# Optimization experiments

Measured on AMD Instinct MI355X. Metric: run time of the kernel, lower is better.

Reference implementation:

```python
import jax, jax.numpy as jnp
import numpy as np

B, N, DIM, H = 8, 1024, 768, 12
D = DIM // H  # head_dim = 64
SCALE = D ** -0.5


def setup_inputs() -> dict:
    key = jax.random.key(0)
    k1, k2, k3, k4 = jax.random.split(key, 4)
    x = jax.random.normal(k1, (B, N, DIM), dtype=jnp.float32)
    # nn.Linear(dim, dim*3, bias=False): weight [3*dim, dim]; y = x @ W^T
    w_qkv = jax.random.normal(k2, (3 * DIM, DIM), dtype=jnp.float32) * (DIM ** -0.5)
    # nn.Linear(dim, dim) with bias
    w_proj = jax.random.normal(k3, (DIM, DIM), dtype=jnp.float32) * (DIM ** -0.5)
    b_proj = jax.random.normal(k4, (DIM,), dtype=jnp.float32) * 0.01
    return {"x": x, "w_qkv": w_qkv, "w_proj": w_proj, "b_proj": b_proj}


def reference(x, w_qkv, w_proj, b_proj):
    b, n, dim = x.shape
    qkv = x @ w_qkv.T  # [b, n, 3*dim]
    # rearrange 'b n (h d qkv) -> qkv b h n d' (qkv innermost in the split)
    qkv = qkv.reshape(b, n, H, D, 3)
    qkv = jnp.transpose(qkv, (4, 0, 2, 1, 3))  # [3, b, h, n, d]
    q, k, v = qkv[0], qkv[1], qkv[2]
    energy = jnp.einsum('bhqd,bhkd->bhqk', q, k) * SCALE
    att = jax.nn.softmax(energy, axis=-1)  # dropout p=0.0 -> identity
    out = jnp.einsum('bhal,bhlv->bhav', att, v)  # [b, h, n, d]
    out = jnp.transpose(out, (0, 2, 1, 3)).reshape(b, n, dim)
    return out @ w_proj.T + b_proj
```

## Files before the change

kernel.cpp:

```cpp
#include <hip/hip_runtime.h>
#include <hip/hip_bf16.h>
#include <stdint.h>

#define NH 12

typedef __attribute__((ext_vector_type(8))) short bf16x8;
typedef __attribute__((ext_vector_type(4))) float f32x4;

static __device__ __forceinline__ ushort f2bf(float f) {
  union { float f; uint32_t u; } v; v.f = f;
  uint32_t r = (v.u + 0x7FFFu + ((v.u >> 16) & 1u)) >> 16;
  return (ushort)r;
}

static __device__ __forceinline__ uint32_t cvtpk(float lo, float hi) {
  uint32_t r;
  asm("v_cvt_pk_bf16_f32 %0, %1, %2" : "=v"(r) : "v"(lo), "v"(hi));
  return r;
}

static __device__ __forceinline__ void gl_lds16(const void* g, void* l) {
  __builtin_amdgcn_global_load_lds(
      (const __attribute__((address_space(1))) uint32_t*)(uintptr_t)g,
      (__attribute__((address_space(3))) uint32_t*)(uintptr_t)l,
      16, 0, 0);
}

static __device__ __forceinline__ f32x4 mfma32(bf16x8 a, bf16x8 b, f32x4 c) {
  return __builtin_amdgcn_mfma_f32_16x16x32_bf16(a, b, c, 0, 0, 0);
}

#define QSCALE 0.1803368801111601f

__global__ __launch_bounds__(256) void k_cvt(const float4* __restrict__ src,
                                             ushort4* __restrict__ dst, int n4) {
  int i = blockIdx.x * blockDim.x + threadIdx.x;
  if (i < n4) {
    float4 v = src[i];
    ushort4 o;
    o.x = f2bf(v.x); o.y = f2bf(v.y); o.z = f2bf(v.z); o.w = f2bf(v.w);
    dst[i] = o;
  }
}

__global__ __launch_bounds__(256) void k_cvt_wq(const float4* __restrict__ src,
                                                ushort4* __restrict__ dst) {
  int i = blockIdx.x * 256 + threadIdx.x;
  if (i >= 2304 * 192) return;
  int ro = i / 192, cc = i - ro * 192;
  int h = ro / 192;
  int rem = ro - h * 192;
  int d = rem / 3;
  int which = rem - d * 3;
  int rn = which * 768 + h * 64 + d;
  float4 v = src[i];
  ushort4 o;
  o.x = f2bf(v.x); o.y = f2bf(v.y); o.z = f2bf(v.z); o.w = f2bf(v.w);
  dst[(size_t)rn * 192 + cc] = o;
}

#define DECL_GEMM_VARS() \
  const int tid = threadIdx.x; \
  const int w = tid >> 6, l = tid & 63, g = l >> 4, c15 = l & 15; \
  const int wm = w >> 1, wn = w & 1; \
  const int dst0 = w * 1024 + l * 16; \
  const int row_s = w * 16 + (l >> 2); \
  const int cg = ((l & 3) ^ ((l >> 3) & 3)) * 8; \
  const int gsw = (g ^ ((c15 >> 1) & 3)) * 8;

#define STAGE(pa, pb, Aptr, Bptr, kk0) do { \
    gl_lds16((Aptr) + (size_t)(m0 + row_s) * 768 + (kk0) + cg, (char*)(pa) + dst0); \
    gl_lds16((Aptr) + (size_t)(m0 + row_s + 64) * 768 + (kk0) + cg, (char*)(pa) + dst0 + 4096); \
    gl_lds16((Bptr) + (size_t)(n0 + row_s) * 768 + (kk0) + cg, (char*)(pb) + dst0); \
    gl_lds16((Bptr) + (size_t)(n0 + row_s + 64) * 768 + (kk0) + cg, (char*)(pb) + dst0 + 4096); \
  } while (0)

#define COMPUTE(pa, pb) do { \
    bf16x8 af[4], bfr[4]; \
    _Pragma("unroll") \
    for (int i = 0; i < 4; i++) { \
      af[i]  = *(const bf16x8*)&(pa)[(wm * 64 + i * 16 + c15) * 32 + gsw]; \
      bfr[i] = *(const bf16x8*)&(pb)[(wn * 64 + i * 16 + c15) * 32 + gsw]; \
    } \
    _Pragma("unroll") \
    for (int mr = 0; mr < 4; mr++) \
      _Pragma("unroll") \
      for (int nr = 0; nr < 4; nr++) \
        acc[mr][nr] = mfma32(af[mr], bfr[nr], acc[mr][nr]); \
  } while (0)

#define WB4 do { __builtin_amdgcn_sched_barrier(0); \
    asm volatile("s_waitcnt vmcnt(4)\n\ts_barrier" ::: "memory"); \
    __builtin_amdgcn_sched_barrier(0); } while (0)
#define WB0 do { __builtin_amdgcn_sched_barrier(0); \
    asm volatile("s_waitcnt vmcnt(0)\n\ts_barrier" ::: "memory"); \
    __builtin_amdgcn_sched_barrier(0); } while (0)
#define PFENCE do { asm volatile("" ::: "memory"); \
    __builtin_amdgcn_sched_barrier(0); } while (0)

#define GEMM_PIPE(Aptr, Bptr) do { \
    STAGE(A0, B0, Aptr, Bptr, 0); \
    PFENCE; \
    STAGE(A1, B1, Aptr, Bptr, 32); \
    WB4; \
    _Pragma("unroll 1") \
    for (int k0 = 0; k0 < 672; k0 += 96) { \
      STAGE(A2, B2, Aptr, Bptr, k0 + 64);  COMPUTE(A0, B0); WB4; \
      STAGE(A0, B0, Aptr, Bptr, k0 + 96);  COMPUTE(A1, B1); WB4; \
      STAGE(A1, B1, Aptr, Bptr, k0 + 128); COMPUTE(A2, B2); WB4; \
    } \
    STAGE(A2, B2, Aptr, Bptr, 736); COMPUTE(A0, B0); WB4; \
    COMPUTE(A1, B1); WB0; \
    COMPUTE(A2, B2); \
  } while (0)

__global__ __launch_bounds__(256, 3) void k_qkv(const ushort* __restrict__ X,
                                                const ushort* __restrict__ W,
                                                ushort* __restrict__ Qb,
                                                ushort* __restrict__ Kf,
                                                ushort* __restrict__ Vf) {
  __shared__ __align__(16) ushort lds[24576];
  const int id = (int)blockIdx.x;
  const int swz = (id & 7) * 144 + (id >> 3);
  const int bx = swz % 18, by = swz / 18;
  const int m0 = by * 128, n0 = bx * 128;
  DECL_GEMM_VARS();

  ushort* A0 = lds;
  ushort* A1 = lds + 4096;
  ushort* A2 = lds + 8192;
  ushort* B0 = lds + 12288;
  ushort* B1 = lds + 16384;
  ushort* B2 = lds + 20480;

  f32x4 acc[4][4] = {};
  GEMM_PIPE(X, W);
  __syncthreads();

  const int type = bx / 6;
  const int cb = (bx % 6) * 128;
  const int h0 = cb >> 6;
  const int b = m0 >> 10, nbase = m0 & 1023, tbase = nbase >> 5;

  if (type == 0) {
#pragma unroll
    for (int nr = 0; nr < 4; nr++) {
      const int colrel = wn * 64 + nr * 16 + c15;
#pragma unroll
      for (int mr = 0; mr < 4; mr++)
#pragma unroll
        for (int r = 0; r < 4; r++) {
          const int mrel = wm * 64 + mr * 16 + 4 * g + r;
          lds[mrel * 128 + colrel] = f2bf(acc[mr][nr][r] * QSCALE);
        }
    }
    __syncthreads();
#pragma unroll
    for (int j = 0; j < 8; j++) {
      const int cid = j * 256 + tid;
      const int n = cid >> 4, coloff = (cid & 15) * 8;
      const int hrel = coloff >> 6, d0q = coloff & 63;
      bf16x8 vv = *(const bf16x8*)&lds[n * 128 + coloff];
      *(bf16x8*)(Qb + ((size_t)(b * NH + h0 + hrel) * 1024 + nbase + n) * 64 + d0q) = vv;
    }
  } else if (type == 1) {
#pragma unroll
    for (int nr = 0; nr < 4; nr++) {
      const int colrel = wn * 64 + nr * 16 + c15;
      const int hrel = colrel >> 6, d = colrel & 63;
      const int gk = (d >> 3) & 3, ek = d & 7, hi = d >> 5;
#pragma unroll
      for (int mr = 0; mr < 4; mr++)
#pragma unroll
        for (int r = 0; r < 4; r++) {
          const int mrel = wm * 64 + mr * 16 + 4 * g + r;
          const int trel = mrel >> 5, kk = mrel & 31;
          const int x = kk >> 3, s = (kk >> 2) & 1, y = kk & 3;
          lds[(hrel * 4 + trel) * 2048 + (2 * s + hi) * 512 +
              (gk * 16 + x * 4 + y) * 8 + ek] = f2bf(acc[mr][nr][r]);
        }
    }
    __syncthreads();
    const int c = tid >> 5, jj = tid & 31;
    ushort* dst = Kf + ((size_t)(b * NH + h0 + (c >> 2)) * 32 + tbase + (c & 3)) * 2048;
    const ushort* srcl = lds + c * 2048;
#pragma unroll
    for (int k2 = 0; k2 < 8; k2++)
      *(bf16x8*)(dst + jj * 8 + k2 * 256) = *(const bf16x8*)(srcl + jj * 8 + k2 * 256);
  } else {
#pragma unroll
    for (int nr = 0; nr < 4; nr++) {
      const int colrel = wn * 64 + nr * 16 + c15;
      const int hrel = colrel >> 6, d = colrel & 63;
      const int dtv = d >> 4, cv = d & 15;
#pragma unroll
      for (int mr = 0; mr < 4; mr++)
#pragma unroll
        for (int r = 0; r < 4; r++) {
          const int mrel = wm * 64 + mr * 16 + 4 * g + r;
          const int trel = mrel >> 5, kk = mrel & 31;
          const int gv = kk >> 3, ev = kk & 7;
          lds[(hrel * 4 + trel) * 2048 + dtv * 512 +
              (gv * 16 + cv) * 8 + ev] = f2bf(acc[mr][nr][r]);
        }
    }
    __syncthreads();
    const int c = tid >> 5, jj = tid & 31;
    ushort* dst = Vf + ((size_t)(b * NH + h0 + (c >> 2)) * 32 + tbase + (c & 3)) * 2048;
    const ushort* srcl = lds + c * 2048;
#pragma unroll
    for (int k2 = 0; k2 < 8; k2++)
      *(bf16x8*)(dst + jj * 8 + k2 * 256) = *(const bf16x8*)(srcl + jj * 8 + k2 * 256);
  }
}

__global__ __launch_bounds__(256, 3) void k_attn(const ushort* __restrict__ Qb,
                                                 const ushort* __restrict__ Kf,
                                                 const ushort* __restrict__ Vf,
                                                 ushort* __restrict__ Ab) {
  const int bh = blockIdx.x;
  const int tid = threadIdx.x;
  const int w = tid >> 6, l = tid & 63, g = l >> 4, c15 = l & 15;
  const int q0 = blockIdx.y * 128 + w * 32;

  bf16x8 qf0a, qf0b, qf1a, qf1b;
  {
    const ushort* qp = Qb + ((size_t)bh * 1024 + q0 + c15) * 64 + g * 8;
    qf0a = *(const bf16x8*)qp;
    qf0b = *(const bf16x8*)(qp + 32);
    qf1a = *(const bf16x8*)(qp + 1024);
    qf1b = *(const bf16x8*)(qp + 1024 + 32);
  }
  const ushort* kfb = Kf + (size_t)bh * 32 * 2048 + l * 8;
  const ushort* vfb = Vf + (size_t)bh * 32 * 2048 + l * 8;

  bf16x8 vones;
#pragma unroll
  for (int j = 0; j < 8; j++) vones[j] = (short)0x3F80;

  f32x4 o0[4] = {}, o1[4] = {};
  f32x4 ol0 = {}, ol1 = {};

  bf16x8 kA[4], vA[4], kB[4], vB[4];
#pragma unroll
  for (int j = 0; j < 4; j++) {
    kA[j] = *(const bf16x8*)(kfb + j * 512);
    vA[j] = *(const bf16x8*)(vfb + j * 512);
  }

#define ATT_BODY(KK, VV) do { \
    f32x4 s00 = {0.f,0.f,0.f,0.f}, s01 = {0.f,0.f,0.f,0.f}; \
    f32x4 s10 = {0.f,0.f,0.f,0.f}, s11 = {0.f,0.f,0.f,0.f}; \
    s00 = mfma32(KK[0], qf0a, s00); s00 = mfma32(KK[1], qf0b, s00); \
    s01 = mfma32(KK[0], qf1a, s01); s01 = mfma32(KK[1], qf1b, s01); \
    s10 = mfma32(KK[2], qf0a, s10); s10 = mfma32(KK[3], qf0b, s10); \
    s11 = mfma32(KK[2], qf1a, s11); s11 = mfma32(KK[3], qf1b, s11); \
    float p0[8], p1[8]; \
    _Pragma("unroll") \
    for (int r = 0; r < 4; r++) { \
      p0[r]     = exp2f(s00[r]); \
      p0[4 + r] = exp2f(s10[r]); \
      p1[r]     = exp2f(s01[r]); \
      p1[4 + r] = exp2f(s11[r]); \
    } \
    union { uint32_t u[4]; bf16x8 v; } pa0, pa1; \
    _Pragma("unroll") \
    for (int j = 0; j < 4; j++) { \
      pa0.u[j] = cvtpk(p0[2 * j], p0[2 * j + 1]); \
      pa1.u[j] = cvtpk(p1[2 * j], p1[2 * j + 1]); \
    } \
    ol0 = mfma32(pa0.v, vones, ol0); \
    ol1 = mfma32(pa1.v, vones, ol1); \
    _Pragma("unroll") \
    for (int dt = 0; dt < 4; dt++) { \
      o0[dt] = mfma32(pa0.v, VV[dt], o0[dt]); \
      o1[dt] = mfma32(pa1.v, VV[dt], o1[dt]); \
    } \
  } while (0)

#pragma unroll 1
  for (int t = 0; t < 32; t += 2) {
    {
      const ushort* kp = kfb + (t + 1) * 2048;
      const ushort* vp = vfb + (t + 1) * 2048;
#pragma unroll
      for (int j = 0; j < 4; j++) {
        kB[j] = *(const bf16x8*)(kp + j * 512);
        vB[j] = *(const bf16x8*)(vp + j * 512);
      }
    }
    ATT_BODY(kA, vA);
    {
      const int tn = (t + 2 < 32) ? (t + 2) : 31;
      const ushort* kp = kfb + tn * 2048;
      const ushort* vp = vfb + tn * 2048;
#pragma unroll
      for (int j = 0; j < 4; j++) {
        kA[j] = *(const bf16x8*)(kp + j * 512);
        vA[j] = *(const bf16x8*)(vp + j * 512);
      }
    }
    ATT_BODY(kB, vB);
  }
#undef ATT_BODY

  float il0[4], il1[4];
#pragma unroll
  for (int r = 0; r < 4; r++) {
    il0[r] = __builtin_amdgcn_rcpf(ol0[r]);
    il1[r] = __builtin_amdgcn_rcpf(ol1[r]);
  }
  const int b = bh / NH, h = bh % NH;
#pragma unroll
  for (int dt = 0; dt < 4; dt++)
#pragma unroll
    for (int r = 0; r < 4; r++) {
      const int n = q0 + 4 * g + r;
      Ab[(size_t)(b * 1024 + n) * 768 + h * 64 + dt * 16 + c15] =
          f2bf(o0[dt][r] * il0[r]);
      Ab[(size_t)(b * 1024 + n + 16) * 768 + h * 64 + dt * 16 + c15] =
          f2bf(o1[dt][r] * il1[r]);
    }
}

__global__ __launch_bounds__(256, 3) void k_proj(const ushort* __restrict__ Ain,
                                                 const ushort* __restrict__ W,
                                                 const float* __restrict__ Bp,
                                                 float* __restrict__ Out) {
  __shared__ __align__(16) ushort lds[24576];
  const int id = (int)blockIdx.x;
  const int swz = (id & 7) * 48 + (id >> 3);
  const int bx = swz % 6, by = swz / 6;
  const int m0 = by * 128, n0 = bx * 128;
  DECL_GEMM_VARS();

  ushort* A0 = lds;
  ushort* A1 = lds + 4096;
  ushort* A2 = lds + 8192;
  ushort* B0 = lds + 12288;
  ushort* B1 = lds + 16384;
  ushort* B2 = lds + 20480;

  f32x4 acc[4][4] = {};
  GEMM_PIPE(Ain, W);

#pragma unroll
  for (int nr = 0; nr < 4; nr++) {
    const int cc = n0 + wn * 64 + nr * 16 + c15;
    const float bias = Bp[cc];
#pragma unroll
    for (int mr = 0; mr < 4; mr++) {
      const int mb = m0 + wm * 64 + mr * 16 + 4 * g;
#pragma unroll
      for (int r = 0; r < 4; r++) {
        const int m = mb + r;
        Out[(size_t)m * 768 + cc] = acc[mr][nr][r] + bias;
      }
    }
  }
}

extern "C" void kernel_launch(void* const* d_in, const int* in_sizes, int n_in,
                              void* d_out, int out_size, void* d_ws, size_t ws_size,
                              hipStream_t stream) {
  const float* X  = (const float*)d_in[0];
  const float* Wq = (const float*)d_in[1];
  const float* Wp = (const float*)d_in[2];
  const float* Bp = (const float*)d_in[3];
  float* Out = (float*)d_out;

  char* ws = (char*)d_ws;
  const size_t SZ = (size_t)96 * 1024 * 64 * sizeof(ushort);
  ushort* Qb  = (ushort*)(ws);
  ushort* Kf  = (ushort*)(ws + SZ);
  ushort* Vf  = (ushort*)(ws + 2 * SZ);
  ushort* Ab  = (ushort*)(ws + 3 * SZ);
  ushort* Xb  = (ushort*)(ws + 4 * SZ);
  ushort* Wqb = (ushort*)(ws + 5 * SZ);
  ushort* Wpb = (ushort*)(ws + 5 * SZ + 2304 * 768 * 2);

  const int nX = 8192 * 768 / 4, nWp = 768 * 768 / 4;
  k_cvt<<<(nX + 255) / 256, 256, 0, stream>>>((const float4*)X, (ushort4*)Xb, nX);
  k_cvt_wq<<<(2304 * 192 + 255) / 256, 256, 0, stream>>>((const float4*)Wq, (ushort4*)Wqb);
  k_cvt<<<(nWp + 255) / 256, 256, 0, stream>>>((const float4*)Wp, (ushort4*)Wpb, nWp);

  k_qkv<<<1152, 256, 0, stream>>>(Xb, Wqb, Qb, Kf, Vf);
  k_attn<<<dim3(96, 8), 256, 0, stream>>>(Qb, Kf, Vf, Ab);
  k_proj<<<384, 256, 0, stream>>>(Ab, Wpb, Bp, Out);
}
```

Measured before the change: 133.1 us.

## Share K/V tiles via LDS triple buffer in attention and fuse conversion kernels

```diff
diff --git a/kernel.cpp b/kernel.cpp
--- a/kernel.cpp
+++ b/kernel.cpp
@@ -32,31 +32,40 @@
 
 #define QSCALE 0.1803368801111601f
 
-__global__ __launch_bounds__(256) void k_cvt(const float4* __restrict__ src,
-                                             ushort4* __restrict__ dst, int n4) {
-  int i = blockIdx.x * blockDim.x + threadIdx.x;
-  if (i < n4) {
-    float4 v = src[i];
+#define N4_X  1572864
+#define N4_WQ 442368
+#define N4_WP 147456
+__global__ __launch_bounds__(256) void k_cvt_all(const float4* __restrict__ X,
+                                                 const float4* __restrict__ Wq,
+                                                 const float4* __restrict__ Wp,
+                                                 ushort4* __restrict__ Xb,
+                                                 ushort4* __restrict__ Wqb,
+                                                 ushort4* __restrict__ Wpb) {
+  int i = blockIdx.x * 256 + threadIdx.x;
+  if (i < N4_X) {
+    float4 v = X[i];
     ushort4 o;
     o.x = f2bf(v.x); o.y = f2bf(v.y); o.z = f2bf(v.z); o.w = f2bf(v.w);
-    dst[i] = o;
-  }
-}
-
-__global__ __launch_bounds__(256) void k_cvt_wq(const float4* __restrict__ src,
-                                                ushort4* __restrict__ dst) {
-  int i = blockIdx.x * 256 + threadIdx.x;
-  if (i >= 2304 * 192) return;
-  int ro = i / 192, cc = i - ro * 192;
-  int h = ro / 192;
-  int rem = ro - h * 192;
-  int d = rem / 3;
-  int which = rem - d * 3;
-  int rn = which * 768 + h * 64 + d;
-  float4 v = src[i];
-  ushort4 o;
-  o.x = f2bf(v.x); o.y = f2bf(v.y); o.z = f2bf(v.z); o.w = f2bf(v.w);
-  dst[(size_t)rn * 192 + cc] = o;
+    Xb[i] = o;
+  } else if (i < N4_X + N4_WQ) {
+    int j = i - N4_X;
+    int ro = j / 192, cc = j - ro * 192;
+    int h = ro / 192;
+    int rem = ro - h * 192;
+    int d = rem / 3;
+    int which = rem - d * 3;
+    int rn = which * 768 + h * 64 + d;
+    float4 v = Wq[j];
+    ushort4 o;
+    o.x = f2bf(v.x); o.y = f2bf(v.y); o.z = f2bf(v.z); o.w = f2bf(v.w);
+    Wqb[(size_t)rn * 192 + cc] = o;
+  } else {
+    int j = i - N4_X - N4_WQ;
+    float4 v = Wp[j];
+    ushort4 o;
+    o.x = f2bf(v.x); o.y = f2bf(v.y); o.z = f2bf(v.z); o.w = f2bf(v.w);
+    Wpb[j] = o;
+  }
 }
 
 #define DECL_GEMM_VARS() \
@@ -91,6 +100,9 @@
 
 #define WB4 do { __builtin_amdgcn_sched_barrier(0); \
     asm volatile("s_waitcnt vmcnt(4)\n\ts_barrier" ::: "memory"); \
+    __builtin_amdgcn_sched_barrier(0); } while (0)
+#define WB2 do { __builtin_amdgcn_sched_barrier(0); \
+    asm volatile("s_waitcnt vmcnt(2)\n\ts_barrier" ::: "memory"); \
     __builtin_amdgcn_sched_barrier(0); } while (0)
 #define WB0 do { __builtin_amdgcn_sched_barrier(0); \
     asm volatile("s_waitcnt vmcnt(0)\n\ts_barrier" ::: "memory"); \
@@ -218,6 +230,7 @@
                                                  const ushort* __restrict__ Kf,
                                                  const ushort* __restrict__ Vf,
                                                  ushort* __restrict__ Ab) {
+  __shared__ __align__(16) ushort kv[3][4096];
   const int bh = blockIdx.x;
   const int tid = threadIdx.x;
   const int w = tid >> 6, l = tid & 63, g = l >> 4, c15 = l & 15;
@@ -231,8 +244,8 @@
     qf1a = *(const bf16x8*)(qp + 1024);
     qf1b = *(const bf16x8*)(qp + 1024 + 32);
   }
-  const ushort* kfb = Kf + (size_t)bh * 32 * 2048 + l * 8;
-  const ushort* vfb = Vf + (size_t)bh * 32 * 2048 + l * 8;
+  const ushort* kgb = Kf + (size_t)bh * 32 * 2048;
+  const ushort* vgb = Vf + (size_t)bh * 32 * 2048;
 
   bf16x8 vones;
 #pragma unroll
@@ -241,20 +254,24 @@
   f32x4 o0[4] = {}, o1[4] = {};
   f32x4 ol0 = {}, ol1 = {};
 
-  bf16x8 kA[4], vA[4], kB[4], vB[4];
-#pragma unroll
-  for (int j = 0; j < 4; j++) {
-    kA[j] = *(const bf16x8*)(kfb + j * 512);
-    vA[j] = *(const bf16x8*)(vfb + j * 512);
-  }
-
-#define ATT_BODY(KK, VV) do { \
+#define STAGE_KV(bi, t) do { \
+    gl_lds16(kgb + (size_t)(t) * 2048 + tid * 8, (char*)kv[bi] + tid * 16); \
+    gl_lds16(vgb + (size_t)(t) * 2048 + tid * 8, (char*)kv[bi] + 4096 + tid * 16); \
+  } while (0)
+
+#define ATT_BODY(bi) do { \
+    const ushort* kp = kv[bi] + l * 8; \
+    const ushort* vp = kv[bi] + 2048 + l * 8; \
+    bf16x8 ka0a = *(const bf16x8*)(kp); \
+    bf16x8 ka0b = *(const bf16x8*)(kp + 512); \
+    bf16x8 ka1a = *(const bf16x8*)(kp + 1024); \
+    bf16x8 ka1b = *(const bf16x8*)(kp + 1536); \
     f32x4 s00 = {0.f,0.f,0.f,0.f}, s01 = {0.f,0.f,0.f,0.f}; \
     f32x4 s10 = {0.f,0.f,0.f,0.f}, s11 = {0.f,0.f,0.f,0.f}; \
-    s00 = mfma32(KK[0], qf0a, s00); s00 = mfma32(KK[1], qf0b, s00); \
-    s01 = mfma32(KK[0], qf1a, s01); s01 = mfma32(KK[1], qf1b, s01); \
-    s10 = mfma32(KK[2], qf0a, s10); s10 = mfma32(KK[3], qf0b, s10); \
-    s11 = mfma32(KK[2], qf1a, s11); s11 = mfma32(KK[3], qf1b, s11); \
+    s00 = mfma32(ka0a, qf0a, s00); s00 = mfma32(ka0b, qf0b, s00); \
+    s01 = mfma32(ka0a, qf1a, s01); s01 = mfma32(ka0b, qf1b, s01); \
+    s10 = mfma32(ka1a, qf0a, s10); s10 = mfma32(ka1b, qf0b, s10); \
+    s11 = mfma32(ka1a, qf1a, s11); s11 = mfma32(ka1b, qf1b, s11); \
     float p0[8], p1[8]; \
     _Pragma("unroll") \
     for (int r = 0; r < 4; r++) { \
@@ -273,36 +290,29 @@
     ol1 = mfma32(pa1.v, vones, ol1); \
     _Pragma("unroll") \
     for (int dt = 0; dt < 4; dt++) { \
-      o0[dt] = mfma32(pa0.v, VV[dt], o0[dt]); \
-      o1[dt] = mfma32(pa1.v, VV[dt], o1[dt]); \
-    } \
-  } while (0)
-
+      bf16x8 vb = *(const bf16x8*)(vp + dt * 512); \
+      o0[dt] = mfma32(pa0.v, vb, o0[dt]); \
+      o1[dt] = mfma32(pa1.v, vb, o1[dt]); \
+    } \
+  } while (0)
+
+  STAGE_KV(0, 0);
+  PFENCE;
+  STAGE_KV(1, 1);
+  WB2;
 #pragma unroll 1
-  for (int t = 0; t < 32; t += 2) {
-    {
-      const ushort* kp = kfb + (t + 1) * 2048;
-      const ushort* vp = vfb + (t + 1) * 2048;
-#pragma unroll
-      for (int j = 0; j < 4; j++) {
-        kB[j] = *(const bf16x8*)(kp + j * 512);
-        vB[j] = *(const bf16x8*)(vp + j * 512);
-      }
-    }
-    ATT_BODY(kA, vA);
-    {
-      const int tn = (t + 2 < 32) ? (t + 2) : 31;
-      const ushort* kp = kfb + tn * 2048;
-      const ushort* vp = vfb + tn * 2048;
-#pragma unroll
-      for (int j = 0; j < 4; j++) {
-        kA[j] = *(const bf16x8*)(kp + j * 512);
-        vA[j] = *(const bf16x8*)(vp + j * 512);
-      }
-    }
-    ATT_BODY(kB, vB);
-  }
+  for (int t = 0; t < 27; t += 3) {
+    STAGE_KV(2, t + 2); ATT_BODY(0); WB2;
+    STAGE_KV(0, t + 3); ATT_BODY(1); WB2;
+    STAGE_KV(1, t + 4); ATT_BODY(2); WB2;
+  }
+  STAGE_KV(2, 29); ATT_BODY(0); WB2;
+  STAGE_KV(0, 30); ATT_BODY(1); WB2;
+  STAGE_KV(1, 31); ATT_BODY(2); WB2;
+  ATT_BODY(0); WB0;
+  ATT_BODY(1);
 #undef ATT_BODY
+#undef STAGE_KV
 
   float il0[4], il1[4];
 #pragma unroll
@@ -379,10 +389,9 @@
   ushort* Wqb = (ushort*)(ws + 5 * SZ);
   ushort* Wpb = (ushort*)(ws + 5 * SZ + 2304 * 768 * 2);
 
-  const int nX = 8192 * 768 / 4, nWp = 768 * 768 / 4;
-  k_cvt<<<(nX + 255) / 256, 256, 0, stream>>>((const float4*)X, (ushort4*)Xb, nX);
-  k_cvt_wq<<<(2304 * 192 + 255) / 256, 256, 0, stream>>>((const float4*)Wq, (ushort4*)Wqb);
-  k_cvt<<<(nWp + 255) / 256, 256, 0, stream>>>((const float4*)Wp, (ushort4*)Wpb, nWp);
+  k_cvt_all<<<(N4_X + N4_WQ + N4_WP) / 256, 256, 0, stream>>>(
+      (const float4*)X, (const float4*)Wq, (const float4*)Wp,
+      (ushort4*)Xb, (ushort4*)Wqb, (ushort4*)Wpb);
 
   k_qkv<<<1152, 256, 0, stream>>>(Xb, Wqb, Qb, Kf, Vf);
   k_attn<<<dim3(96, 8), 256, 0, stream>>>(Qb, Kf, Vf, Ab);
```

After: 108.6 us, median of 3. 18.4% less time.
